# Kernel optimization log

Hardware: AMD Instinct MI355X
Metric: run time of the kernel (lower is better)

The kernel has to match this reference:

```python
import jax, jax.numpy as jnp
import numpy as np
import math

N = 200000      # active voxels
M = 80000       # rule pairs per kernel offset
K = 27          # 3^3 kernel offsets
INC, OUTC = 64, 128   # supernet max channels
RIN, ROUT = 48, 96    # runtime (sampled) channels


def setup_inputs() -> dict:
    key = jax.random.key(0)
    k1, k2, k3, k4 = jax.random.split(key, 4)
    features = jax.random.normal(k1, (N, RIN), dtype=jnp.float32)
    std = 1.0 / math.sqrt(INC * K)  # matches init_weight (non-transposed)
    kernel = jax.random.uniform(k2, (K, INC, OUTC), dtype=jnp.float32,
                                minval=-std, maxval=std)
    in_map = jax.random.randint(k3, (K, M), 0, N, dtype=jnp.int32)
    out_map = jax.random.randint(k4, (K, M), 0, N, dtype=jnp.int32)
    return {"features": features, "kernel": kernel,
            "in_map": in_map, "out_map": out_map,
            "rin": RIN, "rout": ROUT}


def reference(features, kernel, in_map, out_map, rin, rout):
    # Dynamic channel slicing: kernel[:, arange(rin), :][..., arange(rout)]
    w = kernel[:, :rin, :rout]                      # [K, rin, rout]
    # Gather-GEMM-scatter rulebook sparse conv (torchsparse spf.conv3d):
    gathered = features[in_map]                     # [K, M, rin]
    contrib = jnp.einsum('kmi,kio->kmo', gathered, w)  # [K, M, rout]
    out = jnp.zeros((features.shape[0], rout), dtype=features.dtype)
    out = out.at[out_map.reshape(-1)].add(contrib.reshape(-1, rout))
    return out
```

## Files before the change

kernel.cpp:

```cpp
#include <hip/hip_runtime.h>
#include <hip/hip_bf16.h>

#define KK   27
#define MM   80000
#define NN   200000
#define INC  64
#define OUTC 128
#define RIN  48
#define ROUT 96

#define SLICE   40
#define NSLICE  (NN / SLICE)
#define NKEY    (KK * NSLICE)

#define HEPB    4096
#define HBLK    ((MM + HEPB - 1) / HEPB)
#define NC      (NKEY * HBLK)
#define ETOT    (KK * MM)

#define SCHUNK  1024
#define NCB     ((NC + SCHUNK - 1) / SCHUNK)
#define MIDW    11

#define CHUNK   768

typedef __attribute__((ext_vector_type(8))) short bf16x8;
typedef __attribute__((ext_vector_type(4))) float f32x4;

__device__ __forceinline__ float bf2f(short s) {
    return __uint_as_float(((unsigned)(unsigned short)s) << 16);
}

#define FB_BLOCKS_PER_K 200
#define FB_ENTRIES_PER_BLOCK ((MM + FB_BLOCKS_PER_K - 1) / FB_BLOCKS_PER_K)

__global__ __launch_bounds__(192)
void sparse_conv_scatter(const float* __restrict__ feat,
                         const float* __restrict__ w,
                         const int* __restrict__ imap,
                         const int* __restrict__ omap,
                         float* __restrict__ out)
{
    __shared__ float wlds[RIN * ROUT];
    const int k = blockIdx.y;
    const float* wk = w + (size_t)k * INC * OUTC;
    for (int idx = threadIdx.x; idx < RIN * ROUT; idx += 192) {
        int i = idx / ROUT;
        int o = idx - i * ROUT;
        wlds[idx] = wk[i * OUTC + o];
    }
    __syncthreads();

    const int sub = threadIdx.x / 96;
    const int oc  = threadIdx.x % 96;
    const int m0 = blockIdx.x * FB_ENTRIES_PER_BLOCK;
    const int m1 = min(m0 + FB_ENTRIES_PER_BLOCK, MM);
    const int* imk = imap + (size_t)k * MM;
    const int* omk = omap + (size_t)k * MM;

    for (int m = m0 + sub; m < m1; m += 2) {
        const int fin  = imk[m];
        const int fout = omk[m];
        const float4* f4 = (const float4*)(feat + (size_t)fin * RIN);
        float acc = 0.f;
        #pragma unroll
        for (int i4 = 0; i4 < RIN / 4; ++i4) {
            float4 v = f4[i4];
            acc += v.x * wlds[(i4 * 4 + 0) * ROUT + oc];
            acc += v.y * wlds[(i4 * 4 + 1) * ROUT + oc];
            acc += v.z * wlds[(i4 * 4 + 2) * ROUT + oc];
            acc += v.w * wlds[(i4 * 4 + 3) * ROUT + oc];
        }
        atomicAdd(&out[(size_t)fout * ROUT + oc], acc);
    }
}

__global__ __launch_bounds__(256)
void feat_to_bf16(const float* __restrict__ f, __hip_bfloat16* __restrict__ fb)
{
    const size_t i = (size_t)blockIdx.x * 256 + threadIdx.x;
    if (i >= (size_t)NN * RIN / 8) return;
    const float4* p = (const float4*)(f + i * 8);
    float4 a = p[0], b = p[1];
    union { __hip_bfloat16 h[8]; uint4 v; } o;
    o.h[0] = __float2bfloat16(a.x);
    o.h[1] = __float2bfloat16(a.y);
    o.h[2] = __float2bfloat16(a.z);
    o.h[3] = __float2bfloat16(a.w);
    o.h[4] = __float2bfloat16(b.x);
    o.h[5] = __float2bfloat16(b.y);
    o.h[6] = __float2bfloat16(b.z);
    o.h[7] = __float2bfloat16(b.w);
    ((uint4*)fb)[i] = o.v;
}

__global__ __launch_bounds__(64)
void build_wpack(const float* __restrict__ w, __hip_bfloat16* __restrict__ wp)
{
    const int b = blockIdx.x;
    const int k = b / 12;
    const int f = b % 12;
    const int oct = f / 2, ktile = f % 2;
    const int lane = threadIdx.x;
    const int oc    = oct * 16 + (lane & 15);
    const int kbase = ktile * 32 + (lane >> 4) * 8;
    union { __hip_bfloat16 h[8]; uint4 v; } o;
    #pragma unroll
    for (int j = 0; j < 8; ++j) {
        int ki = kbase + j;
        float val = (ki < RIN) ? w[(size_t)k * INC * OUTC + (size_t)ki * OUTC + oc] : 0.f;
        o.h[j] = __float2bfloat16(val);
    }
    ((uint4*)wp)[(size_t)b * 64 + lane] = o.v;
}

__global__ __launch_bounds__(256)
void hist_pass(const int* __restrict__ omap, int* __restrict__ C)
{
    __shared__ int h[NSLICE];
    const int k = blockIdx.y;
    const int blk = blockIdx.x;
    for (int i = threadIdx.x; i < NSLICE; i += 256) h[i] = 0;
    __syncthreads();

    #pragma unroll
    for (int it = 0; it < HEPB / 256; ++it) {
        const int m = blk * HEPB + it * 256 + threadIdx.x;
        if (m < MM) atomicAdd(&h[omap[(size_t)k * MM + m] / SLICE], 1);
    }
    __syncthreads();
    for (int i = threadIdx.x; i < NSLICE; i += 256)
        C[((size_t)k * NSLICE + i) * HBLK + blk] = h[i];
}

__global__ __launch_bounds__(256)
void scan_part2(const int* __restrict__ C, int* __restrict__ S)
{
    __shared__ int sh[256];
    const int t = threadIdx.x;
    const int base = blockIdx.x * SCHUNK + t * 4;
    int s = 0;
    #pragma unroll
    for (int j = 0; j < 4; ++j)
        if (base + j < NC) s += C[base + j];
    sh[t] = s;
    __syncthreads();
    for (int off = 128; off > 0; off >>= 1) {
        if (t < off) sh[t] += sh[t + off];
        __syncthreads();
    }
    if (t == 0) S[blockIdx.x] = sh[0];
}

__global__ __launch_bounds__(256)
void scan_mid(int* __restrict__ S)
{
    __shared__ int sh[256];
    const int t = threadIdx.x;
    int v[MIDW];
    int tot = 0;
    #pragma unroll
    for (int j = 0; j < MIDW; ++j) {
        const int idx = t * MIDW + j;
        v[j] = (idx < NCB) ? S[idx] : 0;
        tot += v[j];
    }
    sh[t] = tot;
    __syncthreads();
    for (int off = 1; off < 256; off <<= 1) {
        int x = (t >= off) ? sh[t - off] : 0;
        __syncthreads();
        sh[t] += x;
        __syncthreads();
    }
    int run = sh[t] - tot;
    #pragma unroll
    for (int j = 0; j < MIDW; ++j) {
        const int idx = t * MIDW + j;
        if (idx < NCB) { const int tv = v[j]; S[idx] = run; run += tv; }
    }
}

__global__ __launch_bounds__(256)
void scan_final2(int* __restrict__ C, const int* __restrict__ S)
{
    __shared__ int sh[256];
    const int t = threadIdx.x;
    const int base = blockIdx.x * SCHUNK + t * 4;
    int v[4];
    int s = 0;
    #pragma unroll
    for (int j = 0; j < 4; ++j) {
        v[j] = (base + j < NC) ? C[base + j] : 0;
        s += v[j];
    }
    sh[t] = s;
    __syncthreads();
    for (int off = 1; off < 256; off <<= 1) {
        int x = (t >= off) ? sh[t - off] : 0;
        __syncthreads();
        sh[t] += x;
        __syncthreads();
    }
    int run = sh[t] - s + S[blockIdx.x];
    #pragma unroll
    for (int j = 0; j < 4; ++j) {
        if (base + j < NC) { C[base + j] = run; run += v[j]; }
    }
}

__global__ __launch_bounds__(256)
void write_elist(const int* __restrict__ omap,
                 const int* __restrict__ imap,
                 const int* __restrict__ Cs,
                 unsigned* __restrict__ elist)
{
    __shared__ int run[NSLICE];
    const int k = blockIdx.y;
    const int blk = blockIdx.x;
    for (int i = threadIdx.x; i < NSLICE; i += 256) run[i] = 0;
    __syncthreads();

    #pragma unroll
    for (int it = 0; it < HEPB / 256; ++it) {
        const int m = blk * HEPB + it * 256 + threadIdx.x;
        if (m < MM) {
            const size_t e = (size_t)k * MM + m;
            const int r = omap[e];
            const int s = r / SLICE;
            const int lr = r - s * SLICE;
            const int rank = atomicAdd(&run[s], 1);
            const int base = Cs[((size_t)k * NSLICE + s) * HBLK + blk];
            elist[base + rank] = (unsigned)imap[e] | ((unsigned)lr << 18);
        }
    }
}

__global__ __launch_bounds__(256)
void stage1_mfma(const __hip_bfloat16* __restrict__ fb,
                 const __hip_bfloat16* __restrict__ wp,
                 const unsigned* __restrict__ elist,
                 const int* __restrict__ Cs,
                 int t, int spr, int capseg,
                 __hip_bfloat16* __restrict__ contrib)
{
    const int k = blockIdx.y;
    const int wid  = threadIdx.x >> 6;
    const int lane = threadIdx.x & 63;
    const int lo = lane & 15, hi = lane >> 4;

    const size_t key0 = (size_t)k * NSLICE + (size_t)t * spr;
    const size_t key1 = key0 + spr;
    const int seg0 = Cs[key0 * HBLK];
    const int seg1 = (key1 < NKEY) ? Cs[key1 * HBLK] : ETOT;
    const int n = seg1 - seg0;
    const int ntiles = (n + 15) >> 4;

    bf16x8 B[12];
    #pragma unroll
    for (int f = 0; f < 12; ++f)
        B[f] = *reinterpret_cast<const bf16x8*>(
            (const char*)wp + (((size_t)k * 12 + f) * 64 + lane) * 16);

    const int wstride = gridDim.x * 4;
    int tile = blockIdx.x * 4 + wid;
    if (tile >= ntiles) return;

    int ea0 = seg0 + tile * 16 + lo;
    unsigned tg = (ea0 < seg1) ? elist[ea0] : 0u;
    int row = (int)(tg & 0x3FFFFu);
    bf16x8 A0 = *reinterpret_cast<const bf16x8*>((const char*)fb + (size_t)row * 96 + hi * 16);
    bf16x8 A1 = *reinterpret_cast<const bf16x8*>((const char*)fb + (size_t)row * 96 + 64 + hi * 16);

    while (tile < ntiles) {
        const int nt_ = tile + wstride;
        bf16x8 nA0, nA1;
        if (nt_ < ntiles) {
            const int ea = seg0 + nt_ * 16 + lo;
            const unsigned ntg = (ea < seg1) ? elist[ea] : 0u;
            const int nrow = (int)(ntg & 0x3FFFFu);
            nA0 = *reinterpret_cast<const bf16x8*>((const char*)fb + (size_t)nrow * 96 + hi * 16);
            nA1 = *reinterpret_cast<const bf16x8*>((const char*)fb + (size_t)nrow * 96 + 64 + hi * 16);
        }

        const int e4 = tile * 16 + hi * 4;
        const size_t sbase = (size_t)k * capseg + e4;
        const bool v0 = (e4 + 0) < n, v1 = (e4 + 1) < n,
                   v2 = (e4 + 2) < n, v3 = (e4 + 3) < n;

        #pragma unroll
        for (int oct = 0; oct < 6; ++oct) {
            f32x4 a = {0.f, 0.f, 0.f, 0.f};
            a = __builtin_amdgcn_mfma_f32_16x16x32_bf16(A0, B[oct * 2 + 0], a, 0, 0, 0);
            a = __builtin_amdgcn_mfma_f32_16x16x32_bf16(A1, B[oct * 2 + 1], a, 0, 0, 0);
            const int oc = oct * 16 + lo;
            if (v0) contrib[(sbase + 0) * ROUT + oc] = __float2bfloat16(a[0]);
            if (v1) contrib[(sbase + 1) * ROUT + oc] = __float2bfloat16(a[1]);
            if (v2) contrib[(sbase + 2) * ROUT + oc] = __float2bfloat16(a[2]);
            if (v3) contrib[(sbase + 3) * ROUT + oc] = __float2bfloat16(a[3]);
        }

        tile = nt_;
        A0 = nA0;
        A1 = nA1;
    }
}

__global__ __launch_bounds__(512)
void stage2_sorted(const __hip_bfloat16* __restrict__ contrib,
                   const unsigned* __restrict__ elist,
                   const int* __restrict__ Cs,
                   int t, int spr, int capseg,
                   float* __restrict__ out)
{
    __shared__ int kb0[KK], klb[KK];
    __shared__ int koff[KK + 1];
    __shared__ int rowcnt[SLICE];
    __shared__ int rowoff[SLICE + 1];
    __shared__ int srcSorted[CHUNK];

    const int sl  = t * spr + blockIdx.x;
    const int tid = threadIdx.x;

    if (tid < KK) {
        const int k = tid;
        const size_t key = (size_t)k * NSLICE + sl;
        const int b0 = Cs[key * HBLK];
        const int b1 = (key + 1 < NKEY) ? Cs[(key + 1) * HBLK] : ETOT;
        const int segb = Cs[((size_t)k * NSLICE + (size_t)t * spr) * HBLK];
        kb0[k]  = b0;
        klb[k]  = k * capseg + (b0 - segb);
        koff[k] = b1 - b0;
    }
    __syncthreads();
    if (tid == 0) {
        int run = 0;
        for (int k = 0; k < KK; ++k) { const int c = koff[k]; koff[k] = run; run += c; }
        koff[KK] = run;
    }
    __syncthreads();
    const int nE = koff[KK];

    const int lr = tid / 12;
    const int g  = tid - lr * 12;
    const bool owner = (tid < SLICE * 12);

    f32x4 accA = {0.f, 0.f, 0.f, 0.f};
    f32x4 accB = {0.f, 0.f, 0.f, 0.f};

    for (int c0 = 0; c0 < nE; c0 += CHUNK) {
        const int ce = min(nE - c0, CHUNK);

        if (tid < SLICE) rowcnt[tid] = 0;
        __syncthreads();

        int myLr[2], myRank[2], mySrc[2];
        int nmine = 0;
        for (int i = tid; i < ce; i += 512) {
            const int ge = c0 + i;
            int lo = 0, hi = KK;
            while (hi - lo > 1) {
                const int mid = (lo + hi) >> 1;
                if (ge >= koff[mid]) lo = mid; else hi = mid;
            }
            const int j = ge - koff[lo];
            const int l = (int)(elist[kb0[lo] + j] >> 18);
            myLr[nmine]   = l;
            mySrc[nmine]  = klb[lo] + j;
            myRank[nmine] = atomicAdd(&rowcnt[l], 1);
            ++nmine;
        }
        __syncthreads();

        if (tid == 0) {
            int run = 0;
            for (int r = 0; r < SLICE; ++r) { rowoff[r] = run; run += rowcnt[r]; }
            rowoff[SLICE] = run;
        }
        __syncthreads();

        for (int q = 0; q < nmine; ++q)
            srcSorted[rowoff[myLr[q]] + myRank[q]] = mySrc[q];
        __syncthreads();

        if (owner) {
            const int j0 = rowoff[lr], j1 = rowoff[lr + 1];
            for (int j = j0; j < j1; ++j) {
                const bf16x8 v = *reinterpret_cast<const bf16x8*>(
                    contrib + (size_t)srcSorted[j] * ROUT + g * 8);
                accA[0] += bf2f(v[0]); accA[1] += bf2f(v[1]);
                accA[2] += bf2f(v[2]); accA[3] += bf2f(v[3]);
                accB[0] += bf2f(v[4]); accB[1] += bf2f(v[5]);
                accB[2] += bf2f(v[6]); accB[3] += bf2f(v[7]);
            }
        }
        __syncthreads();
    }

    if (owner) {
        float4* o = (float4*)(out + ((size_t)sl * SLICE + lr) * ROUT + g * 8);
        float4 x0 = {accA[0], accA[1], accA[2], accA[3]};
        float4 x1 = {accB[0], accB[1], accB[2], accB[3]};
        o[0] = x0; o[1] = x1;
    }
}

extern "C" void kernel_launch(void* const* d_in, const int* in_sizes, int n_in,
                              void* d_out, int out_size, void* d_ws, size_t ws_size,
                              hipStream_t stream)
{
    const float* features = (const float*)d_in[0];
    const float* kernel_w = (const float*)d_in[1];
    const int*   in_map   = (const int*)d_in[2];
    const int*   out_map  = (const int*)d_in[3];
    float*       out      = (float*)d_out;

    const size_t off_C       = 0;
    const size_t off_S       = off_C + (((size_t)NC * 4 + 255) & ~255ul);
    const size_t off_fb      = off_S + (((size_t)NCB * 4 + 255) & ~255ul);
    const size_t off_wp      = off_fb + (size_t)NN * RIN * 2;
    const size_t off_elist   = off_wp + (size_t)KK * 12 * 64 * 16;
    const size_t off_contrib = off_elist + (((size_t)ETOT + 64) * 4);

    int nt = 0, capseg = 0;
    {
        const size_t need1 = off_contrib + (size_t)KK * 80000 * ROUT * 2;
        const size_t need2 = off_contrib + (size_t)KK * 41472 * ROUT * 2;
        const size_t need4 = off_contrib + (size_t)KK * 21504 * ROUT * 2;
        if      (ws_size >= need1) { nt = 1; capseg = 80000; }
        else if (ws_size >= need2) { nt = 2; capseg = 41472; }
        else if (ws_size >= need4) { nt = 4; capseg = 21504; }
    }

    if (nt == 0) {
        hipMemsetAsync(d_out, 0, (size_t)out_size * sizeof(float), stream);
        dim3 grid(FB_BLOCKS_PER_K, KK);
        sparse_conv_scatter<<<grid, 192, 0, stream>>>(features, kernel_w, in_map, out_map, out);
        return;
    }

    const int spr = NSLICE / nt;
    const int s1x = 320 / nt;

    char* ws = (char*)d_ws;
    int*      C     = (int*)(ws + off_C);
    int*      S     = (int*)(ws + off_S);
    __hip_bfloat16* fb = (__hip_bfloat16*)(ws + off_fb);
    __hip_bfloat16* wp = (__hip_bfloat16*)(ws + off_wp);
    unsigned* elist = (unsigned*)(ws + off_elist);
    __hip_bfloat16* contrib = (__hip_bfloat16*)(ws + off_contrib);

    feat_to_bf16<<<(NN * RIN / 8 + 255) / 256, 256, 0, stream>>>(features, fb);
    build_wpack<<<KK * 12, 64, 0, stream>>>(kernel_w, wp);

    {
        dim3 gh(HBLK, KK);
        hist_pass<<<gh, 256, 0, stream>>>(out_map, C);
    }
    scan_part2<<<NCB, 256, 0, stream>>>(C, S);
    scan_mid<<<1, 256, 0, stream>>>(S);
    scan_final2<<<NCB, 256, 0, stream>>>(C, S);
    {
        dim3 gw(HBLK, KK);
        write_elist<<<gw, 256, 0, stream>>>(out_map, in_map, C, elist);
    }

    for (int t = 0; t < nt; ++t) {
        dim3 g1(s1x, KK);
        stage1_mfma<<<g1, 256, 0, stream>>>(fb, wp, elist, C, t, spr, capseg, contrib);
        stage2_sorted<<<spr, 512, 0, stream>>>(contrib, elist, C, t, spr, capseg, out);
    }
}
```

Measured before the change: 407.5 us.

## Deepen gather prefetch to two tiles and force four-pass slicing

The stage-1 gather-GEMM loop now prefetches feature rows two tiles ahead instead of one, to hide more gather latency behind the MFMA work and stores. The host always picks the four-pass split with a smaller contrib buffer, so the intermediate working set is more likely to stay in cache. The stage-1 grid width per pass also shrinks. Risks: higher register pressure, more kernel launches per pass, and out-of-range prefetches that fall back to row 0.

```diff
diff --git a/kernel.cpp b/kernel.cpp
--- a/kernel.cpp
+++ b/kernel.cpp
@@ -263,25 +263,23 @@
             (const char*)wp + (((size_t)k * 12 + f) * 64 + lane) * 16);
 
     const int wstride = gridDim.x * 4;
-    int tile = blockIdx.x * 4 + wid;
-    if (tile >= ntiles) return;
-
-    int ea0 = seg0 + tile * 16 + lo;
-    unsigned tg = (ea0 < seg1) ? elist[ea0] : 0u;
-    int row = (int)(tg & 0x3FFFFu);
-    bf16x8 A0 = *reinterpret_cast<const bf16x8*>((const char*)fb + (size_t)row * 96 + hi * 16);
-    bf16x8 A1 = *reinterpret_cast<const bf16x8*>((const char*)fb + (size_t)row * 96 + 64 + hi * 16);
-
-    while (tile < ntiles) {
-        const int nt_ = tile + wstride;
-        bf16x8 nA0, nA1;
-        if (nt_ < ntiles) {
-            const int ea = seg0 + nt_ * 16 + lo;
-            const unsigned ntg = (ea < seg1) ? elist[ea] : 0u;
-            const int nrow = (int)(ntg & 0x3FFFFu);
-            nA0 = *reinterpret_cast<const bf16x8*>((const char*)fb + (size_t)nrow * 96 + hi * 16);
-            nA1 = *reinterpret_cast<const bf16x8*>((const char*)fb + (size_t)nrow * 96 + 64 + hi * 16);
-        }
+    const int t0 = blockIdx.x * 4 + wid;
+    if (t0 >= ntiles) return;
+
+    auto LOADA = [&](int tile, bf16x8& a0, bf16x8& a1) {
+        const int ea = seg0 + tile * 16 + lo;
+        const unsigned tg = (tile < ntiles && ea < seg1) ? elist[ea] : 0u;
+        const int row = (int)(tg & 0x3FFFFu);
+        a0 = *reinterpret_cast<const bf16x8*>((const char*)fb + (size_t)row * 96 + hi * 16);
+        a1 = *reinterpret_cast<const bf16x8*>((const char*)fb + (size_t)row * 96 + 64 + hi * 16);
+    };
+
+    bf16x8 A0, A1, P0, P1, Q0, Q1;
+    LOADA(t0, A0, A1);
+    LOADA(t0 + wstride, P0, P1);
+
+    for (int tile = t0; tile < ntiles; tile += wstride) {
+        LOADA(tile + 2 * wstride, Q0, Q1);
 
         const int e4 = tile * 16 + hi * 4;
         const size_t sbase = (size_t)k * capseg + e4;
@@ -300,9 +298,8 @@
             if (v3) contrib[(sbase + 3) * ROUT + oc] = __float2bfloat16(a[3]);
         }
 
-        tile = nt_;
-        A0 = nA0;
-        A1 = nA1;
+        A0 = P0; A1 = P1;
+        P0 = Q0; P1 = Q1;
     }
 }
 
@@ -424,12 +421,8 @@
 
     int nt = 0, capseg = 0;
     {
-        const size_t need1 = off_contrib + (size_t)KK * 80000 * ROUT * 2;
-        const size_t need2 = off_contrib + (size_t)KK * 41472 * ROUT * 2;
         const size_t need4 = off_contrib + (size_t)KK * 21504 * ROUT * 2;
-        if      (ws_size >= need1) { nt = 1; capseg = 80000; }
-        else if (ws_size >= need2) { nt = 2; capseg = 41472; }
-        else if (ws_size >= need4) { nt = 4; capseg = 21504; }
+        if (ws_size >= need4) { nt = 4; capseg = 21504; }
     }
 
     if (nt == 0) {
@@ -440,7 +433,7 @@
     }
 
     const int spr = NSLICE / nt;
-    const int s1x = 320 / nt;
+    const int s1x = 240 / nt;
 
     char* ws = (char*)d_ws;
     int*      C     = (int*)(ws + off_C);
```

After: 411.0 us. About the same (+0.9%).
